# Performance work log

Measured on AMD Instinct MI355X. Metric: run time of the kernel, lower is better.

Reference implementation:

```python
import jax, jax.numpy as jnp
import numpy as np

V, E, H = 32000, 512, 1024
ENC = 2 * H  # bidirectional encoder dim
B, S, T = 32, 128, 64  # batch, src len, decode steps (target len = T+1)


def _p(key, shape, scale=0.02):
    return scale * jax.random.normal(key, shape, dtype=jnp.float32)


def setup_inputs() -> dict:
    key = jax.random.key(0)
    ks = jax.random.split(key, 20)
    emb_w = _p(ks[0], (V, E)).at[0].set(0.0)  # padding_idx=0 zeroed
    inp = {
        "encoder_hidden": jax.random.normal(ks[1], (B, H), dtype=jnp.float32),
        "enc_output": jax.random.normal(ks[2], (B, S, ENC), dtype=jnp.float32),
        "src_mask": jnp.ones((B, S), dtype=bool),
        "target_tokens": jax.random.randint(ks[3], (B, T + 1), 0, V),
        "emb_w": emb_w,
        # Bahdanau attention: score = v^T tanh(Wk enc + Wq h)
        "Wk": _p(ks[4], (H, ENC)), "bk": jnp.zeros((H,), jnp.float32),
        "Wq": _p(ks[5], (H, H)), "bq": jnp.zeros((H,), jnp.float32),
        "v": _p(ks[6], (H,)),
        # GRU layer 0: input = embed + context (E + 2H)
        "Wih0": _p(ks[7], (3 * H, E + ENC)), "Whh0": _p(ks[8], (3 * H, H)),
        "bih0": jnp.zeros((3 * H,), jnp.float32), "bhh0": jnp.zeros((3 * H,), jnp.float32),
        # GRU layer 1
        "Wih1": _p(ks[9], (3 * H, H)), "Whh1": _p(ks[10], (3 * H, H)),
        "bih1": jnp.zeros((3 * H,), jnp.float32), "bhh1": jnp.zeros((3 * H,), jnp.float32),
        # bottleneck: (H + 2H + E) -> E, then tied vocab projection emb_w^T
        "Wb": _p(ks[11], (E, H + ENC + E)), "bb": jnp.zeros((E,), jnp.float32),
    }
    return inp


def _gru_cell(x, h, Wih, Whh, bih, bhh):
    gi = x @ Wih.T + bih
    gh = h @ Whh.T + bhh
    ir, iz, inn = jnp.split(gi, 3, axis=-1)
    hr, hz, hn = jnpp_split = jnp.split(gh, 3, axis=-1)
    r = jax.nn.sigmoid(ir + hr)
    z = jax.nn.sigmoid(iz + hz)
    n = jnp.tanh(inn + r * hn)
    return (1.0 - z) * n + z * h


def reference(encoder_hidden, enc_output, src_mask, target_tokens, emb_w,
              Wk, bk, Wq, bq, v, Wih0, Whh0, bih0, bhh0,
              Wih1, Whh1, bih1, bhh1, Wb, bb):
    # precompute encoder-side attention projection [B,S,H]
    enc_proj = jnp.einsum('bsd,hd->bsh', enc_output, Wk) + bk
    h_init = jnp.stack([encoder_hidden, encoder_hidden])  # [2,B,H]
    tokens = target_tokens[:, :-1].T  # [T,B] teacher forcing inputs

    def step(h, tok):
        emb = emb_w[tok]  # [B,E]
        q = h[1] @ Wq.T + bq  # top-layer hidden drives attention
        e = jnp.tanh(enc_proj + q[:, None, :]) @ v  # [B,S]
        e = jnp.where(src_mask, e, -1e9)
        attn = jax.nn.softmax(e, axis=-1)
        ctx = jnp.einsum('bs,bsd->bd', attn, enc_output)  # [B,2H]
        x0 = jnp.concatenate([emb, ctx], axis=-1)
        h0 = _gru_cell(x0, h[0], Wih0, Whh0, bih0, bhh0)
        h1 = _gru_cell(h0, h[1], Wih1, Whh1, bih1, bhh1)
        feat = jnp.concatenate([h1, ctx, emb], axis=-1)
        bott = jnp.tanh(feat @ Wb.T + bb)
        logits = bott @ emb_w.T  # tied vocab projection [B,V]
        return jnp.stack([h0, h1]), (logits, attn)

    _, (logits, attns) = jax.lax.scan(step, h_init, tokens)
    logits = logits.transpose(1, 0, 2)  # [B,T,V]
    preds = jnp.argmax(logits, axis=-1)  # [B,T]
    attns = attns.transpose(1, 0, 2)  # [B,T,S]
    return logits, preds, attns
```

## Files before the change

kernel.cpp:

```cpp
#include <hip/hip_runtime.h>

typedef unsigned int u32;
typedef unsigned long long u64;

constexpr int V = 32000, E = 512, H = 1024, ENC = 2048, B = 32, S = 128, T = 64;
constexpr int NB = 256;

constexpr size_t OFF_ENCPROJ = 0;
constexpr size_t OFF_EMBALL  = OFF_ENCPROJ + (size_t)B * S * H;
constexpr size_t OFF_H0      = OFF_EMBALL + (size_t)T * B * E;
constexpr size_t OFF_H1      = OFF_H0 + (size_t)B * H;
constexpr size_t OFF_QP      = OFF_H1 + (size_t)B * H;
constexpr size_t OFF_GH0P    = OFF_QP + (size_t)2 * B * H;
constexpr size_t OFF_GH1P    = OFF_GH0P + (size_t)2 * B * 3 * H;
constexpr size_t OFF_GI0P    = OFF_GH1P + (size_t)2 * B * 3 * H;
constexpr size_t OFF_GI1P    = OFF_GI0P + (size_t)5 * B * 3 * H;
constexpr size_t OFF_BOTTP   = OFF_GI1P + (size_t)4 * B * 3 * H;
constexpr size_t OFF_BOTTALL = OFF_BOTTP + (size_t)28 * B * E;
constexpr size_t OFF_XCAT0   = OFF_BOTTALL + (size_t)T * B * E;
constexpr size_t OFF_XCAT1   = OFF_XCAT0 + (size_t)B * (E + ENC);
constexpr size_t OFF_EBUF    = OFF_XCAT1 + (size_t)B * (H + ENC + E);
constexpr size_t OFF_PRED    = OFF_EBUF + (size_t)B * S;
constexpr size_t OFF_BAR     = OFF_PRED + (size_t)2 * B * T;

constexpr size_t OUT_LOGITS = 0;
constexpr size_t OUT_PREDS  = (size_t)B * T * V;
constexpr size_t OUT_ATTN   = OUT_PREDS + (size_t)B * T;

__device__ __forceinline__ float cload(const float* p) {
    return __hip_atomic_load(p, __ATOMIC_RELAXED, __HIP_MEMORY_SCOPE_AGENT);
}
__device__ __forceinline__ void cstore(float* p, float v) {
    __hip_atomic_store(p, v, __ATOMIC_RELAXED, __HIP_MEMORY_SCOPE_AGENT);
}

__device__ __forceinline__ void gridbar(u32* bar, u32 target) {
    __syncthreads();
    if (threadIdx.x == 0) {
        __hip_atomic_fetch_add(bar, 1u, __ATOMIC_RELAXED, __HIP_MEMORY_SCOPE_AGENT);
        while (__hip_atomic_load(bar, __ATOMIC_RELAXED, __HIP_MEMORY_SCOPE_AGENT) < target)
            __builtin_amdgcn_s_sleep(2);
    }
    __syncthreads();
}

__device__ __forceinline__ void gtile(
    const float* __restrict__ x, int K, const float* __restrict__ W,
    float* smw, float* smx, int n0, int kb0, int KL,
    float* __restrict__ pout, int Nstr)
{
    const int tid = threadIdx.x;
    const int nl = tid & 63, ks = tid >> 6;
    float acc[32];
#pragma unroll
    for (int m = 0; m < 32; ++m) acc[m] = 0.f;
    const int nchunks = KL >> 7;
    for (int c = 0; c < nchunks; ++c) {
        const int kb = kb0 + c * 128;
        for (int i = 0; i < 4; ++i) {
            const int f = i * 512 + tid;
            const int r = f >> 5, c4 = f & 31;
            *(float4*)(smw + r * 132 + c4 * 4) =
                *(const float4*)(W + (size_t)(n0 + r) * K + kb + c4 * 4);
        }
        for (int i = 0; i < 8; ++i) {
            const int f = i * 512 + tid;
            const int r = f >> 7, cc = f & 127;
            smx[r * 132 + cc] = cload(x + (size_t)r * K + kb + cc);
        }
        __syncthreads();
        const int kof = ks * 16;
        for (int kt = 0; kt < 4; ++kt) {
            const float4 wv = *(const float4*)(smw + nl * 132 + kof + kt * 4);
#pragma unroll
            for (int m = 0; m < 32; ++m) {
                const float4 xv = *(const float4*)(smx + m * 132 + kof + kt * 4);
                acc[m] = fmaf(xv.x, wv.x, acc[m]);
                acc[m] = fmaf(xv.y, wv.y, acc[m]);
                acc[m] = fmaf(xv.z, wv.z, acc[m]);
                acc[m] = fmaf(xv.w, wv.w, acc[m]);
            }
        }
        __syncthreads();
    }
    if (ks >= 4) {
#pragma unroll
        for (int m = 0; m < 32; ++m) smw[(ks - 4) * 2048 + m * 64 + nl] = acc[m];
    }
    __syncthreads();
    if (ks < 4) {
#pragma unroll
        for (int m = 0; m < 32; ++m) acc[m] += smw[ks * 2048 + m * 64 + nl];
    }
    __syncthreads();
    if (ks < 4) {
#pragma unroll
        for (int m = 0; m < 32; ++m) smw[ks * 2048 + m * 64 + nl] = acc[m];
    }
    __syncthreads();
    for (int j = 0; j < 4; ++j) {
        const int o = j * 512 + tid;
        const int mo = o >> 6, n = o & 63;
        float s = smw[mo * 64 + n] + smw[2048 + mo * 64 + n] +
                  smw[4096 + mo * 64 + n] + smw[6144 + mo * 64 + n];
        cstore(pout + (size_t)mo * Nstr + n0 + n, s);
    }
}

__device__ __forceinline__ void gru_comb(
    const float* __restrict__ gip, int gcnt, const float* __restrict__ ghp,
    const float* __restrict__ bih, const float* __restrict__ bhh,
    float* __restrict__ h, float* __restrict__ xdst, int xstride, int i)
{
    const int m = i >> 10, j = i & 1023;
    float gr = bih[j], gz = bih[H + j], gn = bih[2 * H + j];
    for (int k = 0; k < gcnt; ++k) {
        const float* p = gip + ((size_t)k * B + m) * 3 * H + j;
        gr += cload(p); gz += cload(p + H); gn += cload(p + 2 * H);
    }
    float hr = bhh[j], hz = bhh[H + j], hn = bhh[2 * H + j];
    for (int k = 0; k < 2; ++k) {
        const float* p = ghp + ((size_t)k * B + m) * 3 * H + j;
        hr += cload(p); hz += cload(p + H); hn += cload(p + 2 * H);
    }
    float r = 1.f / (1.f + expf(-(gr + hr)));
    float z = 1.f / (1.f + expf(-(gz + hz)));
    float n = tanhf(gn + r * hn);
    float hv = (1.f - z) * n + z * cload(h + i);
    cstore(h + i, hv);
    if (xdst) cstore(xdst + (size_t)m * xstride + j, hv);
}

__device__ __forceinline__ u32 f32_sortable(float f) {
    u32 u = __float_as_uint(f);
    return (u & 0x80000000u) ? ~u : (u | 0x80000000u);
}

__global__ __launch_bounds__(512) void k_mega(
    const float* __restrict__ enc, const float* __restrict__ vvec,
    const float* __restrict__ bq,
    const float* __restrict__ Wq, const float* __restrict__ Whh0,
    const float* __restrict__ Whh1, const float* __restrict__ Wih0,
    const float* __restrict__ Wih1, const float* __restrict__ Wb,
    const float* __restrict__ bih0, const float* __restrict__ bhh0,
    const float* __restrict__ bih1, const float* __restrict__ bhh1,
    const float* __restrict__ bb, float* __restrict__ ws,
    float* __restrict__ out)
{
    __shared__ float smem[64 * 132 + 32 * 132];
    float* smw = smem;
    float* smx = smem + 64 * 132;
    const int bid = blockIdx.x, tid = threadIdx.x;
    u32* bar = (u32*)(ws + OFF_BAR);
    u32 bar_ep = 0;
    float* h0 = ws + OFF_H0;
    float* h1 = ws + OFF_H1;

    for (int t = 0; t < T; ++t) {
        if (bid < 224) {
            const float* Wp; const float* xp; float* op; int N, i;
            if (bid < 32)       { i = bid;       Wp = Wq;   xp = h1; op = ws + OFF_QP;   N = H; }
            else if (bid < 128) { i = bid - 32;  Wp = Whh0; xp = h0; op = ws + OFF_GH0P; N = 3 * H; }
            else                { i = bid - 128; Wp = Whh1; xp = h1; op = ws + OFF_GH1P; N = 3 * H; }
            const int nt = i >> 1, kz = i & 1;
            gtile(xp, H, Wp, smw, smx, nt * 64, kz * 512, 512,
                  op + (size_t)kz * B * N, N);
        }
        ++bar_ep; gridbar(bar, bar_ep * (u32)NB);

        {
            const int b = bid >> 3, sg = bid & 7;
            const int w = tid >> 6, lane = tid & 63;
            float4 q4[4], v4[4];
#pragma unroll
            for (int i = 0; i < 4; ++i) {
                const int d = i * 256 + lane * 4;
                const float4 bq4 = *(const float4*)(bq + d);
                q4[i].x = cload(ws + OFF_QP + (size_t)b * H + d) +
                          cload(ws + OFF_QP + ((size_t)B + b) * H + d) + bq4.x;
                q4[i].y = cload(ws + OFF_QP + (size_t)b * H + d + 1) +
                          cload(ws + OFF_QP + ((size_t)B + b) * H + d + 1) + bq4.y;
                q4[i].z = cload(ws + OFF_QP + (size_t)b * H + d + 2) +
                          cload(ws + OFF_QP + ((size_t)B + b) * H + d + 2) + bq4.z;
                q4[i].w = cload(ws + OFF_QP + (size_t)b * H + d + 3) +
                          cload(ws + OFF_QP + ((size_t)B + b) * H + d + 3) + bq4.w;
                v4[i] = *(const float4*)(vvec + d);
            }
            for (int si = 0; si < 2; ++si) {
                const int s = sg * 16 + w * 2 + si;
                float e = 0.f;
#pragma unroll
                for (int i = 0; i < 4; ++i) {
                    const float4 ep = *(const float4*)(ws + OFF_ENCPROJ +
                        ((size_t)b * S + s) * H + i * 256 + lane * 4);
                    e += v4[i].x * tanhf(ep.x + q4[i].x);
                    e += v4[i].y * tanhf(ep.y + q4[i].y);
                    e += v4[i].z * tanhf(ep.z + q4[i].z);
                    e += v4[i].w * tanhf(ep.w + q4[i].w);
                }
                for (int msk = 1; msk < 64; msk <<= 1) e += __shfl_xor(e, msk);
                if (lane == 0) cstore(ws + OFF_EBUF + (size_t)b * S + s, e);
            }
        }
        ++bar_ep; gridbar(bar, bar_ep * (u32)NB);

        if (bid < 128) {
            const int b = bid >> 2, dg = bid & 3;
            const int w = tid >> 6;
            float ev = (tid < S) ? cload(ws + OFF_EBUF + (size_t)b * S + tid) : -3e38f;
            float mx = ev;
            for (int msk = 1; msk < 64; msk <<= 1) mx = fmaxf(mx, __shfl_xor(mx, msk));
            if (tid < S && (tid & 63) == 0) smw[256 + w] = mx;
            __syncthreads();
            mx = fmaxf(smw[256], smw[257]);
            float ex = (tid < S) ? expf(ev - mx) : 0.f;
            float sm = ex;
            for (int msk = 1; msk < 64; msk <<= 1) sm += __shfl_xor(sm, msk);
            if (tid < S && (tid & 63) == 0) smw[258 + w] = sm;
            __syncthreads();
            const float inv = 1.f / (smw[258] + smw[259]);
            if (tid < S) {
                float a = ex * inv;
                smw[tid] = a;
                if (dg == 0) out[OUT_ATTN + ((size_t)b * T + t) * S + tid] = a;
            }
            __syncthreads();
            const int d = dg * 512 + tid;
            const float* eb = enc + (size_t)b * S * ENC + d;
            float c = 0.f;
            for (int s = 0; s < S; ++s) c = fmaf(smw[s], eb[(size_t)s * ENC], c);
            cstore(ws + OFF_XCAT0 + (size_t)b * (E + ENC) + E + d, c);
            cstore(ws + OFF_XCAT1 + (size_t)b * (H + ENC + E) + H + d, c);
            if (dg == 0) {
                const float e0 = ws[OFF_EMBALL + ((size_t)t * B + b) * E + tid];
                cstore(ws + OFF_XCAT0 + (size_t)b * (E + ENC) + tid, e0);
                cstore(ws + OFF_XCAT1 + (size_t)b * (H + ENC + E) + H + ENC + tid, e0);
            }
        }
        ++bar_ep; gridbar(bar, bar_ep * (u32)NB);

        if (bid < 240) {
            const int nt = bid / 5, kz = bid % 5;
            gtile(ws + OFF_XCAT0, E + ENC, Wih0, smw, smx, nt * 64, kz * 512, 512,
                  ws + OFF_GI0P + (size_t)kz * B * 3 * H, 3 * H);
        }
        ++bar_ep; gridbar(bar, bar_ep * (u32)NB);

        if (bid < 64)
            gru_comb(ws + OFF_GI0P, 5, ws + OFF_GH0P, bih0, bhh0, h0,
                     nullptr, 0, bid * 512 + tid);
        ++bar_ep; gridbar(bar, bar_ep * (u32)NB);

        if (bid < 192) {
            const int nt = bid >> 2, kz = bid & 3;
            gtile(h0, H, Wih1, smw, smx, nt * 64, kz * 256, 256,
                  ws + OFF_GI1P + (size_t)kz * B * 3 * H, 3 * H);
        }
        ++bar_ep; gridbar(bar, bar_ep * (u32)NB);

        if (bid < 64)
            gru_comb(ws + OFF_GI1P, 4, ws + OFF_GH1P, bih1, bhh1, h1,
                     ws + OFF_XCAT1, H + ENC + E, bid * 512 + tid);
        ++bar_ep; gridbar(bar, bar_ep * (u32)NB);

        if (bid < 224) {
            const int nt = bid / 28, kz = bid % 28;
            gtile(ws + OFF_XCAT1, H + ENC + E, Wb, smw, smx, nt * 64, kz * 128, 128,
                  ws + OFF_BOTTP + (size_t)kz * B * E, E);
        }
        ++bar_ep; gridbar(bar, bar_ep * (u32)NB);

        if (bid < 32) {
            const int i = bid * 512 + tid;
            const int n = i & 511;
            float s = bb[n];
            for (int k = 0; k < 28; ++k)
                s += cload(ws + OFF_BOTTP + (size_t)k * B * E + i);
            ws[OFF_BOTTALL + (size_t)t * B * E + i] = tanhf(s);
        }
    }
}

__global__ __launch_bounds__(256) void k_init(float* ws, const float* __restrict__ eh) {
    int i = blockIdx.x * 256 + threadIdx.x;
    if (i < B * H) { ws[OFF_H0 + i] = eh[i]; ws[OFF_H1 + i] = eh[i]; }
    if (i < B * T) ((u64*)(ws + OFF_PRED))[i] = 0ull;
    if (i == 0) *((u32*)(ws + OFF_BAR)) = 0u;
}

__global__ __launch_bounds__(256) void k_emb(float* ws, const int* __restrict__ tok,
                                             const float* __restrict__ emb) {
    int i = blockIdx.x * 256 + threadIdx.x;
    int t = i >> 14, b = (i >> 9) & 31, k = i & 511;
    int token = tok[b * (T + 1) + t];
    ws[OFF_EMBALL + i] = emb[(size_t)token * E + k];
}

__global__ __launch_bounds__(256) void k_encproj(
    const float* __restrict__ x, const float* __restrict__ Wk,
    const float* __restrict__ bk, float* __restrict__ outp)
{
    __shared__ float smem[64 * 132];
    const int tid = threadIdx.x;
    const int nl = tid & 63, ks = tid >> 6;
    const int n0 = blockIdx.x * 64;
    const int m0 = blockIdx.y * 32;
    float acc[32];
#pragma unroll
    for (int m = 0; m < 32; ++m) acc[m] = 0.f;
    for (int c = 0; c < 16; ++c) {
        const int kb = c * 128;
        {
            const int r = tid >> 2, wo = (tid & 3) * 32;
            const float4* src = (const float4*)(Wk + (size_t)(n0 + r) * ENC + kb + wo);
            float4* dst = (float4*)(smem + r * 132 + wo);
            for (int i = 0; i < 8; ++i) dst[i] = src[i];
        }
        __syncthreads();
        const float* xb = x + (size_t)m0 * ENC + kb + ks * 32;
        for (int kt = 0; kt < 8; ++kt) {
            const float4 wv = *(const float4*)(smem + nl * 132 + ks * 32 + kt * 4);
#pragma unroll
            for (int m = 0; m < 32; ++m) {
                const float4 xv = *(const float4*)(xb + (size_t)m * ENC + kt * 4);
                acc[m] = fmaf(xv.x, wv.x, acc[m]);
                acc[m] = fmaf(xv.y, wv.y, acc[m]);
                acc[m] = fmaf(xv.z, wv.z, acc[m]);
                acc[m] = fmaf(xv.w, wv.w, acc[m]);
            }
        }
        __syncthreads();
    }
#pragma unroll
    for (int m = 0; m < 32; ++m) smem[ks * 2048 + m * 64 + nl] = acc[m];
    __syncthreads();
    const int mo = tid >> 3, nb = (tid & 7) * 8;
#pragma unroll
    for (int j = 0; j < 8; ++j) {
        const int n = nb + j;
        float s = smem[mo * 64 + n] + smem[2048 + mo * 64 + n] +
                  smem[4096 + mo * 64 + n] + smem[6144 + mo * 64 + n];
        outp[(size_t)(m0 + mo) * H + n0 + n] = s + bk[n0 + n];
    }
}

__global__ __launch_bounds__(256) void k_vocab(
    const float* __restrict__ bottall, const float* __restrict__ emb,
    float* __restrict__ ws, float* __restrict__ out)
{
    __shared__ float smem[64 * 132];
    const int tid = threadIdx.x;
    const int nl = tid & 63, ks = tid >> 6;
    const int v0 = blockIdx.x * 64;
    for (int subm = 0; subm < 8; ++subm) {
        const int m0 = blockIdx.y * 256 + subm * 32;
        float acc[32];
#pragma unroll
        for (int m = 0; m < 32; ++m) acc[m] = 0.f;
        for (int c = 0; c < 4; ++c) {
            const int kb = c * 128;
            {
                const int r = tid >> 2, wo = (tid & 3) * 32;
                const float4* src = (const float4*)(emb + (size_t)(v0 + r) * E + kb + wo);
                float4* dst = (float4*)(smem + r * 132 + wo);
                for (int i = 0; i < 8; ++i) dst[i] = src[i];
            }
            __syncthreads();
            const float* xb = bottall + (size_t)m0 * E + kb + ks * 32;
            for (int kt = 0; kt < 8; ++kt) {
                const float4 wv = *(const float4*)(smem + nl * 132 + ks * 32 + kt * 4);
#pragma unroll
                for (int m = 0; m < 32; ++m) {
                    const float4 xv = *(const float4*)(xb + (size_t)m * E + kt * 4);
                    acc[m] = fmaf(xv.x, wv.x, acc[m]);
                    acc[m] = fmaf(xv.y, wv.y, acc[m]);
                    acc[m] = fmaf(xv.z, wv.z, acc[m]);
                    acc[m] = fmaf(xv.w, wv.w, acc[m]);
                }
            }
            __syncthreads();
        }
#pragma unroll
        for (int m = 0; m < 32; ++m) smem[ks * 2048 + m * 64 + nl] = acc[m];
        __syncthreads();
        const int mo = tid >> 3, nb2 = (tid & 7) * 8;
        const int m = m0 + mo;
        const int tt = m >> 5, bb2 = m & 31;
        float bestv = -3e38f; u32 besti = 0;
#pragma unroll
        for (int j = 0; j < 8; ++j) {
            const int n = nb2 + j;
            float s2 = smem[mo * 64 + n] + smem[2048 + mo * 64 + n] +
                       smem[4096 + mo * 64 + n] + smem[6144 + mo * 64 + n];
            out[OUT_LOGITS + ((size_t)bb2 * T + tt) * V + v0 + n] = s2;
            if (s2 > bestv) { bestv = s2; besti = (u32)(v0 + n); }
        }
        u64 key = ((u64)f32_sortable(bestv) << 32) | (u64)(0xFFFFFFFFu - besti);
        for (int msk = 1; msk < 8; msk <<= 1) {
            u32 lo = (u32)key, hi = (u32)(key >> 32);
            lo = __shfl_xor(lo, msk);
            hi = __shfl_xor(hi, msk);
            u64 o = ((u64)hi << 32) | lo;
            if (o > key) key = o;
        }
        if ((tid & 7) == 0)
            atomicMax((u64*)(ws + OFF_PRED) + (size_t)bb2 * T + tt, key);
        __syncthreads();
    }
}

__global__ __launch_bounds__(256) void k_predfin(const float* __restrict__ ws,
                                                 float* __restrict__ out) {
    int i = blockIdx.x * 256 + threadIdx.x;
    u64 key = ((const u64*)(ws + OFF_PRED))[i];
    out[OUT_PREDS + i] = (float)(0xFFFFFFFFu - (u32)key);
}

extern "C" void kernel_launch(void* const* d_in, const int* in_sizes, int n_in,
                              void* d_out, int out_size, void* d_ws, size_t ws_size,
                              hipStream_t stream) {
    const float* enc_hidden = (const float*)d_in[0];
    const float* enc_out    = (const float*)d_in[1];
    const int*   tokens     = (const int*)d_in[3];
    const float* emb_w      = (const float*)d_in[4];
    const float* Wk   = (const float*)d_in[5];
    const float* bk   = (const float*)d_in[6];
    const float* Wq   = (const float*)d_in[7];
    const float* bq   = (const float*)d_in[8];
    const float* vvec = (const float*)d_in[9];
    const float* Wih0 = (const float*)d_in[10];
    const float* Whh0 = (const float*)d_in[11];
    const float* bih0 = (const float*)d_in[12];
    const float* bhh0 = (const float*)d_in[13];
    const float* Wih1 = (const float*)d_in[14];
    const float* Whh1 = (const float*)d_in[15];
    const float* bih1 = (const float*)d_in[16];
    const float* bhh1 = (const float*)d_in[17];
    const float* Wb   = (const float*)d_in[18];
    const float* bb   = (const float*)d_in[19];
    float* ws  = (float*)d_ws;
    float* out = (float*)d_out;

    k_init<<<128, 256, 0, stream>>>(ws, enc_hidden);
    k_emb<<<4096, 256, 0, stream>>>(ws, tokens, emb_w);
    k_encproj<<<dim3(16, 128), 256, 0, stream>>>(enc_out, Wk, bk, ws + OFF_ENCPROJ);
    k_mega<<<NB, 512, 0, stream>>>(enc_out, vvec, bq, Wq, Whh0, Whh1,
                                   Wih0, Wih1, Wb, bih0, bhh0, bih1, bhh1, bb,
                                   ws, out);
    k_vocab<<<dim3(500, 8), 256, 0, stream>>>(ws + OFF_BOTTALL, emb_w, ws, out);
    k_predfin<<<8, 256, 0, stream>>>(ws, out);
}
```

Baseline: 18.86 ms.

## Restructure decoder megakernel: precompute embedding GEMMs, fuse attention, overlap bottleneck

The embedding contributions to the layer-0 input gates and to the bottleneck are now computed for all timesteps up front in batched GEMMs, with the output buffer used as scratch. The per-step megakernel is reorganised so each batch row's attention scores, softmax and context run in a single block, which removes two grid barriers per step. The bottleneck GEMM for step t-1 is overlapped with the next step's query projection using a partial barrier. The GEMM tiles gain register double-buffering, and the vocab kernel moves to 512 threads with a wider argmax reduction. Together these aim to cut grid-wide synchronisation and serial per-step work, at the cost of more complex barrier logic and reuse of output memory as temporary storage.

```diff
diff --git a/kernel.cpp b/kernel.cpp
--- a/kernel.cpp
+++ b/kernel.cpp
@@ -11,21 +11,21 @@
 constexpr size_t OFF_H0      = OFF_EMBALL + (size_t)T * B * E;
 constexpr size_t OFF_H1      = OFF_H0 + (size_t)B * H;
 constexpr size_t OFF_QP      = OFF_H1 + (size_t)B * H;
-constexpr size_t OFF_GH0P    = OFF_QP + (size_t)2 * B * H;
+constexpr size_t OFF_GH0P    = OFF_QP + (size_t)4 * B * H;
 constexpr size_t OFF_GH1P    = OFF_GH0P + (size_t)2 * B * 3 * H;
 constexpr size_t OFF_GI0P    = OFF_GH1P + (size_t)2 * B * 3 * H;
-constexpr size_t OFF_GI1P    = OFF_GI0P + (size_t)5 * B * 3 * H;
+constexpr size_t OFF_GI1P    = OFF_GI0P + (size_t)4 * B * 3 * H;
 constexpr size_t OFF_BOTTP   = OFF_GI1P + (size_t)4 * B * 3 * H;
-constexpr size_t OFF_BOTTALL = OFF_BOTTP + (size_t)28 * B * E;
-constexpr size_t OFF_XCAT0   = OFF_BOTTALL + (size_t)T * B * E;
-constexpr size_t OFF_XCAT1   = OFF_XCAT0 + (size_t)B * (E + ENC);
-constexpr size_t OFF_EBUF    = OFF_XCAT1 + (size_t)B * (H + ENC + E);
-constexpr size_t OFF_PRED    = OFF_EBUF + (size_t)B * S;
+constexpr size_t OFF_BOTTALL = OFF_BOTTP + (size_t)24 * B * E;
+constexpr size_t OFF_XCAT    = OFF_BOTTALL + (size_t)T * B * E;
+constexpr size_t OFF_PRED    = OFF_XCAT + (size_t)B * (H + ENC);
 constexpr size_t OFF_BAR     = OFF_PRED + (size_t)2 * B * T;
 
 constexpr size_t OUT_LOGITS = 0;
 constexpr size_t OUT_PREDS  = (size_t)B * T * V;
 constexpr size_t OUT_ATTN   = OUT_PREDS + (size_t)B * T;
+constexpr size_t OUT_GIEMB  = 0;
+constexpr size_t OUT_BBEMB  = (size_t)T * B * 3 * H;
 
 __device__ __forceinline__ float cload(const float* p) {
     return __hip_atomic_load(p, __ATOMIC_RELAXED, __HIP_MEMORY_SCOPE_AGENT);
@@ -44,9 +44,22 @@
     __syncthreads();
 }
 
+__device__ __forceinline__ void pbar_sync(u32* bar, u32 target, bool wait) {
+    __syncthreads();
+    if (threadIdx.x == 0) {
+        __hip_atomic_fetch_add(bar, 1u, __ATOMIC_RELAXED, __HIP_MEMORY_SCOPE_AGENT);
+        if (wait)
+            while (__hip_atomic_load(bar, __ATOMIC_RELAXED, __HIP_MEMORY_SCOPE_AGENT) < target)
+                __builtin_amdgcn_s_sleep(2);
+    }
+    __syncthreads();
+}
+
 __device__ __forceinline__ void gtile(
-    const float* __restrict__ x, int K, const float* __restrict__ W,
-    float* smw, float* smx, int n0, int kb0, int KL,
+    const float* __restrict__ x, int xstride,
+    const float* __restrict__ W, int wstride,
+    float* smw, float* smx,
+    int n0, int kb0, int nchunks,
     float* __restrict__ pout, int Nstr)
 {
     const int tid = threadIdx.x;
@@ -54,22 +67,49 @@
     float acc[32];
 #pragma unroll
     for (int m = 0; m < 32; ++m) acc[m] = 0.f;
-    const int nchunks = KL >> 7;
+
+    float4 wreg[4];
+    float  xreg[8];
+    {
+        const int kb = kb0;
+#pragma unroll
+        for (int i = 0; i < 4; ++i) {
+            const int f = i * 512 + tid, r = f >> 5, c4 = f & 31;
+            wreg[i] = *(const float4*)(W + (size_t)(n0 + r) * wstride + kb + c4 * 4);
+        }
+#pragma unroll
+        for (int i = 0; i < 8; ++i) {
+            const int f = i * 512 + tid, r = f >> 7, cc = f & 127;
+            xreg[i] = cload(x + (size_t)r * xstride + kb + cc);
+        }
+#pragma unroll
+        for (int i = 0; i < 4; ++i) {
+            const int f = i * 512 + tid, r = f >> 5, c4 = f & 31;
+            *(float4*)(smw + r * 132 + c4 * 4) = wreg[i];
+        }
+#pragma unroll
+        for (int i = 0; i < 8; ++i) {
+            const int f = i * 512 + tid, r = f >> 7, cc = f & 127;
+            smx[r * 132 + cc] = xreg[i];
+        }
+    }
     for (int c = 0; c < nchunks; ++c) {
-        const int kb = kb0 + c * 128;
-        for (int i = 0; i < 4; ++i) {
-            const int f = i * 512 + tid;
-            const int r = f >> 5, c4 = f & 31;
-            *(float4*)(smw + r * 132 + c4 * 4) =
-                *(const float4*)(W + (size_t)(n0 + r) * K + kb + c4 * 4);
-        }
-        for (int i = 0; i < 8; ++i) {
-            const int f = i * 512 + tid;
-            const int r = f >> 7, cc = f & 127;
-            smx[r * 132 + cc] = cload(x + (size_t)r * K + kb + cc);
-        }
-        __syncthreads();
+        __syncthreads();
+        if (c + 1 < nchunks) {
+            const int kb = kb0 + (c + 1) * 128;
+#pragma unroll
+            for (int i = 0; i < 4; ++i) {
+                const int f = i * 512 + tid, r = f >> 5, c4 = f & 31;
+                wreg[i] = *(const float4*)(W + (size_t)(n0 + r) * wstride + kb + c4 * 4);
+            }
+#pragma unroll
+            for (int i = 0; i < 8; ++i) {
+                const int f = i * 512 + tid, r = f >> 7, cc = f & 127;
+                xreg[i] = cload(x + (size_t)r * xstride + kb + cc);
+            }
+        }
         const int kof = ks * 16;
+#pragma unroll
         for (int kt = 0; kt < 4; ++kt) {
             const float4 wv = *(const float4*)(smw + nl * 132 + kof + kt * 4);
 #pragma unroll
@@ -82,6 +122,18 @@
             }
         }
         __syncthreads();
+        if (c + 1 < nchunks) {
+#pragma unroll
+            for (int i = 0; i < 4; ++i) {
+                const int f = i * 512 + tid, r = f >> 5, c4 = f & 31;
+                *(float4*)(smw + r * 132 + c4 * 4) = wreg[i];
+            }
+#pragma unroll
+            for (int i = 0; i < 8; ++i) {
+                const int f = i * 512 + tid, r = f >> 7, cc = f & 127;
+                smx[r * 132 + cc] = xreg[i];
+            }
+        }
     }
     if (ks >= 4) {
 #pragma unroll
@@ -98,9 +150,9 @@
         for (int m = 0; m < 32; ++m) smw[ks * 2048 + m * 64 + nl] = acc[m];
     }
     __syncthreads();
+#pragma unroll
     for (int j = 0; j < 4; ++j) {
-        const int o = j * 512 + tid;
-        const int mo = o >> 6, n = o & 63;
+        const int o = j * 512 + tid, mo = o >> 6, n = o & 63;
         float s = smw[mo * 64 + n] + smw[2048 + mo * 64 + n] +
                   smw[4096 + mo * 64 + n] + smw[6144 + mo * 64 + n];
         cstore(pout + (size_t)mo * Nstr + n0 + n, s);
@@ -108,12 +160,17 @@
 }
 
 __device__ __forceinline__ void gru_comb(
-    const float* __restrict__ gip, int gcnt, const float* __restrict__ ghp,
+    const float* __restrict__ gip, int gcnt, const float* gie,
+    const float* __restrict__ ghp,
     const float* __restrict__ bih, const float* __restrict__ bhh,
-    float* __restrict__ h, float* __restrict__ xdst, int xstride, int i)
+    float* __restrict__ h, float* xdst, int i)
 {
     const int m = i >> 10, j = i & 1023;
     float gr = bih[j], gz = bih[H + j], gn = bih[2 * H + j];
+    if (gie) {
+        const float* gp = gie + (size_t)m * 3 * H + j;
+        gr += gp[0]; gz += gp[H]; gn += gp[2 * H];
+    }
     for (int k = 0; k < gcnt; ++k) {
         const float* p = gip + ((size_t)k * B + m) * 3 * H + j;
         gr += cload(p); gz += cload(p + H); gn += cload(p + 2 * H);
@@ -128,12 +185,24 @@
     float n = tanhf(gn + r * hn);
     float hv = (1.f - z) * n + z * cload(h + i);
     cstore(h + i, hv);
-    if (xdst) cstore(xdst + (size_t)m * xstride + j, hv);
+    if (xdst) cstore(xdst + (size_t)m * (H + ENC) + j, hv);
 }
 
 __device__ __forceinline__ u32 f32_sortable(float f) {
     u32 u = __float_as_uint(f);
     return (u & 0x80000000u) ? ~u : (u | 0x80000000u);
+}
+
+__device__ __forceinline__ void bott_fin(float* ws, const float* bbemb,
+                                         const float* __restrict__ bb,
+                                         int t, int bid, int tid)
+{
+    const int i = (bid - 64) * 512 + tid;
+    const int n = i & 511;
+    float s = bb[n] + bbemb[(size_t)t * B * E + i];
+    for (int k = 0; k < 24; ++k)
+        s += cload(ws + OFF_BOTTP + (size_t)k * B * E + i);
+    ws[OFF_BOTTALL + (size_t)t * B * E + i] = tanhf(s);
 }
 
 __global__ __launch_bounds__(512) void k_mega(
@@ -144,140 +213,152 @@
     const float* __restrict__ Wih1, const float* __restrict__ Wb,
     const float* __restrict__ bih0, const float* __restrict__ bhh0,
     const float* __restrict__ bih1, const float* __restrict__ bhh1,
-    const float* __restrict__ bb, float* __restrict__ ws,
-    float* __restrict__ out)
+    const float* __restrict__ bb,
+    const float* giemb, const float* bbemb,
+    float* __restrict__ ws, float* out)
 {
-    __shared__ float smem[64 * 132 + 32 * 132];
+    __shared__ float smem[96 * 132];
     float* smw = smem;
     float* smx = smem + 64 * 132;
     const int bid = blockIdx.x, tid = threadIdx.x;
-    u32* bar = (u32*)(ws + OFF_BAR);
-    u32 bar_ep = 0;
-    float* h0 = ws + OFF_H0;
-    float* h1 = ws + OFF_H1;
+    u32* gbar = (u32*)(ws + OFF_BAR);
+    u32* pbar = gbar + 1;
+    u32 g_ep = 0, p_ep = 0;
+    float* h0   = ws + OFF_H0;
+    float* h1   = ws + OFF_H1;
+    float* xcat = ws + OFF_XCAT;
 
     for (int t = 0; t < T; ++t) {
-        if (bid < 224) {
-            const float* Wp; const float* xp; float* op; int N, i;
-            if (bid < 32)       { i = bid;       Wp = Wq;   xp = h1; op = ws + OFF_QP;   N = H; }
-            else if (bid < 128) { i = bid - 32;  Wp = Whh0; xp = h0; op = ws + OFF_GH0P; N = 3 * H; }
-            else                { i = bid - 128; Wp = Whh1; xp = h1; op = ws + OFF_GH1P; N = 3 * H; }
-            const int nt = i >> 1, kz = i & 1;
-            gtile(xp, H, Wp, smw, smx, nt * 64, kz * 512, 512,
-                  op + (size_t)kz * B * N, N);
-        }
-        ++bar_ep; gridbar(bar, bar_ep * (u32)NB);
-
-        {
-            const int b = bid >> 3, sg = bid & 7;
-            const int w = tid >> 6, lane = tid & 63;
-            float4 q4[4], v4[4];
-#pragma unroll
-            for (int i = 0; i < 4; ++i) {
-                const int d = i * 256 + lane * 4;
-                const float4 bq4 = *(const float4*)(bq + d);
-                q4[i].x = cload(ws + OFF_QP + (size_t)b * H + d) +
-                          cload(ws + OFF_QP + ((size_t)B + b) * H + d) + bq4.x;
-                q4[i].y = cload(ws + OFF_QP + (size_t)b * H + d + 1) +
-                          cload(ws + OFF_QP + ((size_t)B + b) * H + d + 1) + bq4.y;
-                q4[i].z = cload(ws + OFF_QP + (size_t)b * H + d + 2) +
-                          cload(ws + OFF_QP + ((size_t)B + b) * H + d + 2) + bq4.z;
-                q4[i].w = cload(ws + OFF_QP + (size_t)b * H + d + 3) +
-                          cload(ws + OFF_QP + ((size_t)B + b) * H + d + 3) + bq4.w;
-                v4[i] = *(const float4*)(vvec + d);
-            }
-            for (int si = 0; si < 2; ++si) {
-                const int s = sg * 16 + w * 2 + si;
-                float e = 0.f;
-#pragma unroll
-                for (int i = 0; i < 4; ++i) {
-                    const float4 ep = *(const float4*)(ws + OFF_ENCPROJ +
-                        ((size_t)b * S + s) * H + i * 256 + lane * 4);
-                    e += v4[i].x * tanhf(ep.x + q4[i].x);
-                    e += v4[i].y * tanhf(ep.y + q4[i].y);
-                    e += v4[i].z * tanhf(ep.z + q4[i].z);
-                    e += v4[i].w * tanhf(ep.w + q4[i].w);
+        if (bid < 64) {
+            const int nt = bid >> 2, kz = bid & 3;
+            gtile(h1, H, Wq, H, smw, smx, nt * 64, kz * 256, 2,
+                  ws + OFF_QP + (size_t)kz * B * H, H);
+        } else if (t > 0) {
+            const int i = bid - 64, nt = i / 24, kz = i % 24;
+            gtile(xcat, H + ENC, Wb, H + ENC + E, smw, smx, nt * 64, kz * 128, 1,
+                  ws + OFF_BOTTP + (size_t)kz * B * E, E);
+            ++p_ep;
+            const bool s9 = (bid < 96);
+            pbar_sync(pbar, p_ep * 192u, s9);
+            if (s9) bott_fin(ws, bbemb, bb, t - 1, bid, tid);
+        }
+        ++g_ep; gridbar(gbar, g_ep * (u32)NB);
+
+        if (bid < 32) {
+            const int b = bid;
+            float* q_lds = smx;
+#pragma unroll
+            for (int r = 0; r < 2; ++r) {
+                const int d = r * 512 + tid;
+                float q = bq[d];
+#pragma unroll
+                for (int k = 0; k < 4; ++k)
+                    q += cload(ws + OFF_QP + ((size_t)k * B + b) * H + d);
+                q_lds[d] = q;
+            }
+            __syncthreads();
+            {
+                const int w = tid >> 6, lane = tid & 63;
+                float vreg[16], qreg[16];
+#pragma unroll
+                for (int j = 0; j < 16; ++j) {
+                    const int d = lane + 64 * j;
+                    vreg[j] = vvec[d];
+                    qreg[j] = q_lds[d];
                 }
-                for (int msk = 1; msk < 64; msk <<= 1) e += __shfl_xor(e, msk);
-                if (lane == 0) cstore(ws + OFF_EBUF + (size_t)b * S + s, e);
-            }
-        }
-        ++bar_ep; gridbar(bar, bar_ep * (u32)NB);
-
-        if (bid < 128) {
-            const int b = bid >> 2, dg = bid & 3;
-            const int w = tid >> 6;
-            float ev = (tid < S) ? cload(ws + OFF_EBUF + (size_t)b * S + tid) : -3e38f;
-            float mx = ev;
-            for (int msk = 1; msk < 64; msk <<= 1) mx = fmaxf(mx, __shfl_xor(mx, msk));
-            if (tid < S && (tid & 63) == 0) smw[256 + w] = mx;
+                for (int si = 0; si < 16; ++si) {
+                    const int s = w * 16 + si;
+                    const float* ep = ws + OFF_ENCPROJ + ((size_t)b * S + s) * H;
+                    float e = 0.f;
+#pragma unroll
+                    for (int j = 0; j < 16; ++j)
+                        e += vreg[j] * tanhf(ep[lane + 64 * j] + qreg[j]);
+                    for (int msk = 1; msk < 64; msk <<= 1) e += __shfl_xor(e, msk);
+                    if (lane == 0) smem[s] = e;
+                }
+            }
             __syncthreads();
-            mx = fmaxf(smw[256], smw[257]);
-            float ex = (tid < S) ? expf(ev - mx) : 0.f;
-            float sm = ex;
-            for (int msk = 1; msk < 64; msk <<= 1) sm += __shfl_xor(sm, msk);
-            if (tid < S && (tid & 63) == 0) smw[258 + w] = sm;
+            {
+                float ev = (tid < S) ? smem[tid] : -3e38f;
+                float mx = ev;
+                for (int msk = 1; msk < 64; msk <<= 1) mx = fmaxf(mx, __shfl_xor(mx, msk));
+                if (tid < S && (tid & 63) == 0) smem[160 + (tid >> 6)] = mx;
+                __syncthreads();
+                mx = fmaxf(smem[160], smem[161]);
+                float ex = (tid < S) ? expf(ev - mx) : 0.f;
+                float sm = ex;
+                for (int msk = 1; msk < 64; msk <<= 1) sm += __shfl_xor(sm, msk);
+                if (tid < S && (tid & 63) == 0) smem[162 + (tid >> 6)] = sm;
+                __syncthreads();
+                const float inv = 1.f / (smem[162] + smem[163]);
+                if (tid < S) {
+                    const float a = ex * inv;
+                    smem[192 + tid] = a;
+                    out[OUT_ATTN + ((size_t)b * T + t) * S + tid] = a;
+                }
+            }
             __syncthreads();
-            const float inv = 1.f / (smw[258] + smw[259]);
-            if (tid < S) {
-                float a = ex * inv;
-                smw[tid] = a;
-                if (dg == 0) out[OUT_ATTN + ((size_t)b * T + t) * S + tid] = a;
-            }
-            __syncthreads();
-            const int d = dg * 512 + tid;
-            const float* eb = enc + (size_t)b * S * ENC + d;
-            float c = 0.f;
-            for (int s = 0; s < S; ++s) c = fmaf(smw[s], eb[(size_t)s * ENC], c);
-            cstore(ws + OFF_XCAT0 + (size_t)b * (E + ENC) + E + d, c);
-            cstore(ws + OFF_XCAT1 + (size_t)b * (H + ENC + E) + H + d, c);
-            if (dg == 0) {
-                const float e0 = ws[OFF_EMBALL + ((size_t)t * B + b) * E + tid];
-                cstore(ws + OFF_XCAT0 + (size_t)b * (E + ENC) + tid, e0);
-                cstore(ws + OFF_XCAT1 + (size_t)b * (H + ENC + E) + H + ENC + tid, e0);
-            }
-        }
-        ++bar_ep; gridbar(bar, bar_ep * (u32)NB);
-
-        if (bid < 240) {
-            const int nt = bid / 5, kz = bid % 5;
-            gtile(ws + OFF_XCAT0, E + ENC, Wih0, smw, smx, nt * 64, kz * 512, 512,
-                  ws + OFF_GI0P + (size_t)kz * B * 3 * H, 3 * H);
-        }
-        ++bar_ep; gridbar(bar, bar_ep * (u32)NB);
-
-        if (bid < 64)
-            gru_comb(ws + OFF_GI0P, 5, ws + OFF_GH0P, bih0, bhh0, h0,
-                     nullptr, 0, bid * 512 + tid);
-        ++bar_ep; gridbar(bar, bar_ep * (u32)NB);
+            {
+                float c0 = 0.f, c1 = 0.f, c2 = 0.f, c3 = 0.f;
+                const float* eb = enc + (size_t)b * S * ENC;
+                for (int s = 0; s < S; ++s) {
+                    const float a = smem[192 + s];
+                    const float* row = eb + (size_t)s * ENC;
+                    c0 = fmaf(a, row[tid], c0);
+                    c1 = fmaf(a, row[512 + tid], c1);
+                    c2 = fmaf(a, row[1024 + tid], c2);
+                    c3 = fmaf(a, row[1536 + tid], c3);
+                }
+                float* cx = xcat + (size_t)b * (H + ENC) + H;
+                cstore(cx + tid, c0);
+                cstore(cx + 512 + tid, c1);
+                cstore(cx + 1024 + tid, c2);
+                cstore(cx + 1536 + tid, c3);
+            }
+        } else if (bid < 128) {
+            const int i = bid - 32, nt = i >> 1, kz = i & 1;
+            gtile(h0, H, Whh0, H, smw, smx, nt * 64, kz * 512, 4,
+                  ws + OFF_GH0P + (size_t)kz * B * 3 * H, 3 * H);
+        } else if (bid < 224) {
+            const int i = bid - 128, nt = i >> 1, kz = i & 1;
+            gtile(h1, H, Whh1, H, smw, smx, nt * 64, kz * 512, 4,
+                  ws + OFF_GH1P + (size_t)kz * B * 3 * H, 3 * H);
+        }
+        ++g_ep; gridbar(gbar, g_ep * (u32)NB);
 
         if (bid < 192) {
             const int nt = bid >> 2, kz = bid & 3;
-            gtile(h0, H, Wih1, smw, smx, nt * 64, kz * 256, 256,
+            gtile(xcat + H, H + ENC, Wih0 + E, E + ENC, smw, smx,
+                  nt * 64, kz * 512, 4,
+                  ws + OFF_GI0P + (size_t)kz * B * 3 * H, 3 * H);
+        }
+        ++g_ep; gridbar(gbar, g_ep * (u32)NB);
+
+        if (bid < 64)
+            gru_comb(ws + OFF_GI0P, 4, giemb + (size_t)t * B * 3 * H,
+                     ws + OFF_GH0P, bih0, bhh0, h0, nullptr, bid * 512 + tid);
+        ++g_ep; gridbar(gbar, g_ep * (u32)NB);
+
+        if (bid < 192) {
+            const int nt = bid >> 2, kz = bid & 3;
+            gtile(h0, H, Wih1, H, smw, smx, nt * 64, kz * 256, 2,
                   ws + OFF_GI1P + (size_t)kz * B * 3 * H, 3 * H);
         }
-        ++bar_ep; gridbar(bar, bar_ep * (u32)NB);
+        ++g_ep; gridbar(gbar, g_ep * (u32)NB);
 
         if (bid < 64)
-            gru_comb(ws + OFF_GI1P, 4, ws + OFF_GH1P, bih1, bhh1, h1,
-                     ws + OFF_XCAT1, H + ENC + E, bid * 512 + tid);
-        ++bar_ep; gridbar(bar, bar_ep * (u32)NB);
-
-        if (bid < 224) {
-            const int nt = bid / 28, kz = bid % 28;
-            gtile(ws + OFF_XCAT1, H + ENC + E, Wb, smw, smx, nt * 64, kz * 128, 128,
-                  ws + OFF_BOTTP + (size_t)kz * B * E, E);
-        }
-        ++bar_ep; gridbar(bar, bar_ep * (u32)NB);
-
-        if (bid < 32) {
-            const int i = bid * 512 + tid;
-            const int n = i & 511;
-            float s = bb[n];
-            for (int k = 0; k < 28; ++k)
-                s += cload(ws + OFF_BOTTP + (size_t)k * B * E + i);
-            ws[OFF_BOTTALL + (size_t)t * B * E + i] = tanhf(s);
-        }
+            gru_comb(ws + OFF_GI1P, 4, nullptr,
+                     ws + OFF_GH1P, bih1, bhh1, h1, xcat, bid * 512 + tid);
+        ++g_ep; gridbar(gbar, g_ep * (u32)NB);
+    }
+    if (bid >= 64) {
+        const int i = bid - 64, nt = i / 24, kz = i % 24;
+        gtile(xcat, H + ENC, Wb, H + ENC + E, smw, smx, nt * 64, kz * 128, 1,
+              ws + OFF_BOTTP + (size_t)kz * B * E, E);
+        ++p_ep;
+        const bool s9 = (bid < 96);
+        pbar_sync(pbar, p_ep * 192u, s9);
+        if (s9) bott_fin(ws, bbemb, bb, T - 1, bid, tid);
     }
 }
 
@@ -285,7 +366,7 @@
     int i = blockIdx.x * 256 + threadIdx.x;
     if (i < B * H) { ws[OFF_H0 + i] = eh[i]; ws[OFF_H1 + i] = eh[i]; }
     if (i < B * T) ((u64*)(ws + OFF_PRED))[i] = 0ull;
-    if (i == 0) *((u32*)(ws + OFF_BAR)) = 0u;
+    if (i < 2) ((u32*)(ws + OFF_BAR))[i] = 0u;
 }
 
 __global__ __launch_bounds__(256) void k_emb(float* ws, const int* __restrict__ tok,
@@ -296,9 +377,10 @@
     ws[OFF_EMBALL + i] = emb[(size_t)token * E + k];
 }
 
-__global__ __launch_bounds__(256) void k_encproj(
-    const float* __restrict__ x, const float* __restrict__ Wk,
-    const float* __restrict__ bk, float* __restrict__ outp)
+__global__ __launch_bounds__(256) void k_pre_gemm(
+    const float* __restrict__ x, int xstride,
+    const float* __restrict__ W, int wstride,
+    int nchunks, const float* bias, float* outp, int ostride)
 {
     __shared__ float smem[64 * 132];
     const int tid = threadIdx.x;
@@ -308,21 +390,21 @@
     float acc[32];
 #pragma unroll
     for (int m = 0; m < 32; ++m) acc[m] = 0.f;
-    for (int c = 0; c < 16; ++c) {
+    for (int c = 0; c < nchunks; ++c) {
         const int kb = c * 128;
         {
             const int r = tid >> 2, wo = (tid & 3) * 32;
-            const float4* src = (const float4*)(Wk + (size_t)(n0 + r) * ENC + kb + wo);
+            const float4* src = (const float4*)(W + (size_t)(n0 + r) * wstride + kb + wo);
             float4* dst = (float4*)(smem + r * 132 + wo);
             for (int i = 0; i < 8; ++i) dst[i] = src[i];
         }
         __syncthreads();
-        const float* xb = x + (size_t)m0 * ENC + kb + ks * 32;
+        const float* xb = x + (size_t)m0 * xstride + kb + ks * 32;
         for (int kt = 0; kt < 8; ++kt) {
             const float4 wv = *(const float4*)(smem + nl * 132 + ks * 32 + kt * 4);
 #pragma unroll
             for (int m = 0; m < 32; ++m) {
-                const float4 xv = *(const float4*)(xb + (size_t)m * ENC + kt * 4);
+                const float4 xv = *(const float4*)(xb + (size_t)m * xstride + kt * 4);
                 acc[m] = fmaf(xv.x, wv.x, acc[m]);
                 acc[m] = fmaf(xv.y, wv.y, acc[m]);
                 acc[m] = fmaf(xv.z, wv.z, acc[m]);
@@ -340,35 +422,37 @@
         const int n = nb + j;
         float s = smem[mo * 64 + n] + smem[2048 + mo * 64 + n] +
                   smem[4096 + mo * 64 + n] + smem[6144 + mo * 64 + n];
-        outp[(size_t)(m0 + mo) * H + n0 + n] = s + bk[n0 + n];
-    }
-}
-
-__global__ __launch_bounds__(256) void k_vocab(
+        if (bias) s += bias[n0 + n];
+        outp[(size_t)(m0 + mo) * ostride + n0 + n] = s;
+    }
+}
+
+__global__ __launch_bounds__(512) void k_vocab(
     const float* __restrict__ bottall, const float* __restrict__ emb,
     float* __restrict__ ws, float* __restrict__ out)
 {
     __shared__ float smem[64 * 132];
-    const int tid = threadIdx.x;
-    const int nl = tid & 63, ks = tid >> 6;
+    const int tid = threadIdx.x, nl = tid & 63, ks = tid >> 6;
     const int v0 = blockIdx.x * 64;
-    for (int subm = 0; subm < 8; ++subm) {
-        const int m0 = blockIdx.y * 256 + subm * 32;
+    for (int subm = 0; subm < 16; ++subm) {
+        const int m0 = blockIdx.y * 512 + subm * 32;
         float acc[32];
 #pragma unroll
         for (int m = 0; m < 32; ++m) acc[m] = 0.f;
         for (int c = 0; c < 4; ++c) {
             const int kb = c * 128;
-            {
-                const int r = tid >> 2, wo = (tid & 3) * 32;
-                const float4* src = (const float4*)(emb + (size_t)(v0 + r) * E + kb + wo);
-                float4* dst = (float4*)(smem + r * 132 + wo);
-                for (int i = 0; i < 8; ++i) dst[i] = src[i];
+#pragma unroll
+            for (int i = 0; i < 4; ++i) {
+                const int f = i * 512 + tid, r = f >> 5, c4 = f & 31;
+                *(float4*)(smem + r * 132 + c4 * 4) =
+                    *(const float4*)(emb + (size_t)(v0 + r) * E + kb + c4 * 4);
             }
             __syncthreads();
-            const float* xb = bottall + (size_t)m0 * E + kb + ks * 32;
-            for (int kt = 0; kt < 8; ++kt) {
-                const float4 wv = *(const float4*)(smem + nl * 132 + ks * 32 + kt * 4);
+            const int kof = ks * 16;
+            const float* xb = bottall + (size_t)m0 * E + kb + kof;
+#pragma unroll
+            for (int kt = 0; kt < 4; ++kt) {
+                const float4 wv = *(const float4*)(smem + nl * 132 + kof + kt * 4);
 #pragma unroll
                 for (int m = 0; m < 32; ++m) {
                     const float4 xv = *(const float4*)(xb + (size_t)m * E + kt * 4);
@@ -380,31 +464,36 @@
             }
             __syncthreads();
         }
-#pragma unroll
-        for (int m = 0; m < 32; ++m) smem[ks * 2048 + m * 64 + nl] = acc[m];
-        __syncthreads();
-        const int mo = tid >> 3, nb2 = (tid & 7) * 8;
-        const int m = m0 + mo;
-        const int tt = m >> 5, bb2 = m & 31;
-        float bestv = -3e38f; u32 besti = 0;
-#pragma unroll
-        for (int j = 0; j < 8; ++j) {
-            const int n = nb2 + j;
-            float s2 = smem[mo * 64 + n] + smem[2048 + mo * 64 + n] +
-                       smem[4096 + mo * 64 + n] + smem[6144 + mo * 64 + n];
-            out[OUT_LOGITS + ((size_t)bb2 * T + tt) * V + v0 + n] = s2;
-            if (s2 > bestv) { bestv = s2; besti = (u32)(v0 + n); }
-        }
-        u64 key = ((u64)f32_sortable(bestv) << 32) | (u64)(0xFFFFFFFFu - besti);
-        for (int msk = 1; msk < 8; msk <<= 1) {
-            u32 lo = (u32)key, hi = (u32)(key >> 32);
-            lo = __shfl_xor(lo, msk);
-            hi = __shfl_xor(hi, msk);
-            u64 o = ((u64)hi << 32) | lo;
-            if (o > key) key = o;
-        }
-        if ((tid & 7) == 0)
-            atomicMax((u64*)(ws + OFF_PRED) + (size_t)bb2 * T + tt, key);
+        if (ks >= 4) {
+#pragma unroll
+            for (int m = 0; m < 32; ++m) smem[(ks - 4) * 2048 + m * 64 + nl] = acc[m];
+        }
+        __syncthreads();
+        if (ks < 4) {
+#pragma unroll
+            for (int m = 0; m < 32; ++m) acc[m] += smem[ks * 2048 + m * 64 + nl];
+        }
+        __syncthreads();
+        if (ks < 4) {
+#pragma unroll
+            for (int m = 0; m < 32; ++m) smem[ks * 2048 + m * 64 + nl] = acc[m];
+        }
+        __syncthreads();
+#pragma unroll
+        for (int j = 0; j < 4; ++j) {
+            const int o = j * 512 + tid, mo = o >> 6, n = o & 63;
+            float s = smem[mo * 64 + n] + smem[2048 + mo * 64 + n] +
+                      smem[4096 + mo * 64 + n] + smem[6144 + mo * 64 + n];
+            const int mrow = m0 + mo, tt = mrow >> 5, b2 = mrow & 31;
+            out[OUT_LOGITS + ((size_t)b2 * T + tt) * V + v0 + n] = s;
+            u64 key = ((u64)f32_sortable(s) << 32) | (u64)(0xFFFFFFFFu - (u32)(v0 + n));
+            for (int msk = 1; msk < 64; msk <<= 1) {
+                u64 o2 = __shfl_xor(key, msk);
+                if (o2 > key) key = o2;
+            }
+            if (nl == 0)
+                atomicMax((u64*)(ws + OFF_PRED) + (size_t)b2 * T + tt, key);
+        }
         __syncthreads();
     }
 }
@@ -441,12 +530,22 @@
     float* ws  = (float*)d_ws;
     float* out = (float*)d_out;
 
+    float* giemb = out + OUT_GIEMB;
+    float* bbemb = out + OUT_BBEMB;
+
     k_init<<<128, 256, 0, stream>>>(ws, enc_hidden);
     k_emb<<<4096, 256, 0, stream>>>(ws, tokens, emb_w);
-    k_encproj<<<dim3(16, 128), 256, 0, stream>>>(enc_out, Wk, bk, ws + OFF_ENCPROJ);
+    k_pre_gemm<<<dim3(16, 128), 256, 0, stream>>>(
+        enc_out, ENC, Wk, ENC, 16, bk, ws + OFF_ENCPROJ, H);
+    k_pre_gemm<<<dim3(48, 64), 256, 0, stream>>>(
+        ws + OFF_EMBALL, E, Wih0, E + ENC, 4, nullptr, giemb, 3 * H);
+    k_pre_gemm<<<dim3(8, 64), 256, 0, stream>>>(
+        ws + OFF_EMBALL, E, Wb + (H + ENC), H + ENC + E, 4, nullptr, bbemb, E);
+
     k_mega<<<NB, 512, 0, stream>>>(enc_out, vvec, bq, Wq, Whh0, Whh1,
                                    Wih0, Wih1, Wb, bih0, bhh0, bih1, bhh1, bb,
-                                   ws, out);
-    k_vocab<<<dim3(500, 8), 256, 0, stream>>>(ws + OFF_BOTTALL, emb_w, ws, out);
+                                   giemb, bbemb, ws, out);
+
+    k_vocab<<<dim3(500, 4), 512, 0, stream>>>(ws + OFF_BOTTALL, emb_w, ws, out);
     k_predfin<<<8, 256, 0, stream>>>(ws, out);
 }
```

Result: slower. 64.86 ms (median of 3 runs) (+243.9%).
